# Kernel optimization log

Measured on AMD Instinct MI355X. Metric: run time of the kernel, lower is better.

Reference implementation:

```python
import jax, jax.numpy as jnp
import numpy as np

B, N, R, DIM = 4, 1024, 5, 1024
H, DH = 16, 64
ALPHA = 128.0
# FLAGS.fix_attention=True, a_sim=False: q * (dim_head**-0.5 * alpha**-1) * mult**-0.5
SCALE = (DH ** -0.5) * (1.0 / ALPHA) * (R ** -0.5)
EPS = 1e-5


def layernorm(x, g):
    mean = jnp.mean(x, axis=-1, keepdims=True)
    var = jnp.mean((x - mean) ** 2, axis=-1, keepdims=True)  # unbiased=False
    return (x - mean) * jax.lax.rsqrt(var + EPS) * g


def setup_inputs() -> dict:
    key = jax.random.key(0)
    ks = jax.random.split(key, 8)
    x = jax.random.normal(ks[0], (B, N, R, DIM), dtype=jnp.float32)
    mask = jax.random.bernoulli(ks[1], 0.9, (B, N))
    g_in = jnp.ones((DIM,), dtype=jnp.float32)
    Wq = jax.random.normal(ks[2], (DIM, H * DH), dtype=jnp.float32) * 0.02
    Wkv = jax.random.normal(ks[3], (DIM, 2 * DH), dtype=jnp.float32) * 0.02
    null_kv = jax.random.normal(ks[4], (2, DH), dtype=jnp.float32)
    Wout = jax.random.normal(ks[5], (H * DH, DIM), dtype=jnp.float32) * 0.02
    g_out = jnp.ones((DIM,), dtype=jnp.float32)
    return {"x": x, "mask": mask, "g_in": g_in, "Wq": Wq, "Wkv": Wkv,
            "null_kv": null_kv, "Wout": Wout, "g_out": g_out}


def reference(x, mask, g_in, Wq, Wkv, null_kv, Wout, g_out):
    # context defaults to the UN-normalized x (set before norm in the original)
    context = x
    xn = layernorm(x, g_in)                               # [b,n,r,dim]
    q = jnp.einsum('bnrc,ce->bnre', xn, Wq)               # [b,n,r,h*d]
    q = q.reshape(B, N, R, H, DH).transpose(0, 3, 1, 2, 4)  # b h n r d
    q = q * SCALE
    kv = jnp.einsum('bnrc,ce->bnre', context, Wkv)        # [b,n,r,2d] (multi-query: 1 kv head)
    k, v = kv[..., :DH], kv[..., DH:]                     # [b,n,r,d]
    # null kv token prepended along the j (sequence) axis, repeated over r
    nk = jnp.broadcast_to(null_kv[0], (B, 1, R, DH))
    nv = jnp.broadcast_to(null_kv[1], (B, 1, R, DH))
    k = jnp.concatenate([nk, k], axis=1)                  # [b,n+1,r,d]
    v = jnp.concatenate([nv, v], axis=1)
    sim = jnp.einsum('bhird,bjrd->bhij', q, k)            # [b,h,n,n+1]
    big = jnp.finfo(sim.dtype).max
    maskp = jnp.pad(mask, ((0, 0), (1, 0)), constant_values=True)  # null token always visible
    sim = jnp.where(maskp[:, None, None, :], sim, -big)
    # pb-relax: subtract detached row max, rescale by alpha
    sim = sim - jax.lax.stop_gradient(jnp.max(sim, axis=-1, keepdims=True))
    attn = jax.nn.softmax(sim * ALPHA, axis=-1)
    out = jnp.einsum('bhij,bjrd->bhird', attn, v)         # b h n r d
    out = out.transpose(0, 2, 3, 1, 4).reshape(B, N, R, H * DH)
    out = jnp.einsum('bnre,eo->bnro', out, Wout)
    return layernorm(out, g_out)
```

## Files before the change

kernel.cpp:

```cpp
#include <hip/hip_runtime.h>

#define B_   4
#define N_   1024
#define R_   5
#define DIM_ 1024
#define H_   16
#define DH_  64
#define NJ   1056
#define CDIM 320
#define MROWS (B_*N_*R_)

typedef unsigned int u32;
typedef unsigned short u16;
typedef __attribute__((ext_vector_type(8))) short bf16x8;
typedef __attribute__((ext_vector_type(4))) float f32x4;
typedef __attribute__((ext_vector_type(16))) float f32x16;

constexpr float SCALEA_ = (float)(0.05590169943749474 * 1.4426950408889634);

__device__ __forceinline__ u16 f2bf(float f) {
  u32 u = __builtin_bit_cast(u32, f);
  u32 r = (u + 0x7fffu + ((u >> 16) & 1u)) >> 16;
  return (u16)r;
}
__device__ __forceinline__ u32 pack2(float lo, float hi) {
  return (u32)f2bf(lo) | ((u32)f2bf(hi) << 16);
}
__device__ __forceinline__ void gld_lds16(void* lds, const void* g) {
  __builtin_amdgcn_global_load_lds((const __attribute__((address_space(1))) u32*)g,
                                   (__attribute__((address_space(3))) u32*)lds, 16, 0, 0);
}

__global__ void mask_detect(const u32* __restrict__ m, int* __restrict__ flag) {
  int t = threadIdx.x;
  int fl = 0;
  for (int i = t; i < 1024; i += 256) {
    u32 wv = m[i];
    if (wv == 0x3f800000u) fl |= 4;
    else if (wv > 1u) fl |= 2;
    if ((i & 1) && wv == 1u) fl |= 1;
  }
  if (fl) atomicOr(flag, fl);
}

__global__ void build_bias(const void* __restrict__ mask, const int* __restrict__ flag,
                           float* __restrict__ biasg) {
  int idx = blockIdx.x * 256 + threadIdx.x;
  if (idx >= B_ * NJ) return;
  int b = idx / NJ, j = idx % NJ;
  int mv;
  if (j == 0) mv = 1;
  else if (j > N_) mv = 0;
  else {
    int fb = flag[0];
    int mode = (fb & 4) ? 2 : ((fb & 2) ? 1 : ((fb & 1) ? 0 : 3));
    int mi = b * N_ + (j - 1);
    if (mode == 0)      mv = ((const int*)mask)[mi] != 0;
    else if (mode == 1) mv = ((const unsigned char*)mask)[mi] != 0;
    else if (mode == 2) mv = ((const float*)mask)[mi] != 0.0f;
    else                mv = ((const int*)mask)[mi * 2] != 0;
  }
  biasg[idx] = mv ? 0.0f : -__builtin_inff();
}

__global__ void kvfill(const float* __restrict__ nullkv, u16* __restrict__ kg, u16* __restrict__ vTg) {
  int idx = blockIdx.x * 256 + threadIdx.x;
  if (idx >= B_ * 32 * CDIM) return;
  int c  = idx % CDIM;
  int jj = (idx / CDIM) & 31;
  int b  = idx / (CDIM * 32);
  int j  = (jj == 0) ? 0 : (1024 + jj);
  u16 kvv, vvv;
  if (jj == 0) { kvv = f2bf(nullkv[c & 63]); vvv = f2bf(nullkv[64 + (c & 63)]); }
  else         { kvv = 0; vvv = 0; }
  kg [(size_t)(b * NJ + j) * CDIM + c] = kvv;
  vTg[(((size_t)b * 33 + (j >> 5)) * CDIM + c) * 32 + (j & 31)] = vvv;
}

__global__ __launch_bounds__(256) void transpose_cast(const float* __restrict__ W,
                                                      u16* __restrict__ WT, int K, int Nn) {
  __shared__ float tile[32][33];
  int tx = threadIdx.x & 31, ty = threadIdx.x >> 5;
  int n0 = blockIdx.x * 32, k0 = blockIdx.y * 32;
  #pragma unroll
  for (int e = 0; e < 4; ++e)
    tile[ty + e * 8][tx] = W[(size_t)(k0 + ty + e * 8) * Nn + n0 + tx];
  __syncthreads();
  #pragma unroll
  for (int e = 0; e < 4; ++e)
    WT[(size_t)(n0 + ty + e * 8) * K + k0 + tx] = f2bf(tile[tx][ty + e * 8]);
}

__global__ __launch_bounds__(256) void ln_in(const float* __restrict__ x, const float* __restrict__ gin,
                                             u16* __restrict__ xn, u16* __restrict__ xb) {
  const size_t row = blockIdx.x;
  const int t = threadIdx.x, w = t >> 6, lane = t & 63;
  const float* xr = x + row * 1024;
  f32x4 v = *(const f32x4*)(xr + t * 4);
  float s = v[0] + v[1] + v[2] + v[3];
  #pragma unroll
  for (int o = 1; o < 64; o <<= 1) s += __shfl_xor(s, o);
  __shared__ float red[8];
  if (lane == 0) red[w] = s;
  __syncthreads();
  float mean = (red[0] + red[1] + red[2] + red[3]) * (1.0f / 1024.0f);
  f32x4 d;
  float ss = 0.f;
  #pragma unroll
  for (int e = 0; e < 4; ++e) { d[e] = v[e] - mean; ss += d[e] * d[e]; }
  #pragma unroll
  for (int o = 1; o < 64; o <<= 1) ss += __shfl_xor(ss, o);
  if (lane == 0) red[4 + w] = ss;
  __syncthreads();
  float var = (red[4] + red[5] + red[6] + red[7]) * (1.0f / 1024.0f);
  float rs = rsqrtf(var + 1e-5f);
  f32x4 gv = *(const f32x4*)(gin + t * 4);
  uint2 o1, o2;
  o1.x = pack2(d[0] * rs * gv[0], d[1] * rs * gv[1]);
  o1.y = pack2(d[2] * rs * gv[2], d[3] * rs * gv[3]);
  o2.x = pack2(v[0], v[1]);
  o2.y = pack2(v[2], v[3]);
  *(uint2*)(xn + row * 1024 + t * 4) = o1;
  *(uint2*)(xb + row * 1024 + t * 4) = o2;
}

__global__ __launch_bounds__(256) void ln_out(const u16* __restrict__ yb, const float* __restrict__ gout,
                                              float* __restrict__ out) {
  const size_t row = blockIdx.x;
  const int t = threadIdx.x, w = t >> 6, lane = t & 63;
  uint2 raw = *(const uint2*)(yb + row * 1024 + t * 4);
  f32x4 v;
  v[0] = __builtin_bit_cast(float, (raw.x & 0xffffu) << 16);
  v[1] = __builtin_bit_cast(float, (raw.x & 0xffff0000u));
  v[2] = __builtin_bit_cast(float, (raw.y & 0xffffu) << 16);
  v[3] = __builtin_bit_cast(float, (raw.y & 0xffff0000u));
  float s = v[0] + v[1] + v[2] + v[3];
  #pragma unroll
  for (int o = 1; o < 64; o <<= 1) s += __shfl_xor(s, o);
  __shared__ float red[8];
  if (lane == 0) red[w] = s;
  __syncthreads();
  float mean = (red[0] + red[1] + red[2] + red[3]) * (1.0f / 1024.0f);
  f32x4 d;
  float ss = 0.f;
  #pragma unroll
  for (int e = 0; e < 4; ++e) { d[e] = v[e] - mean; ss += d[e] * d[e]; }
  #pragma unroll
  for (int o = 1; o < 64; o <<= 1) ss += __shfl_xor(ss, o);
  if (lane == 0) red[4 + w] = ss;
  __syncthreads();
  float var = (red[4] + red[5] + red[6] + red[7]) * (1.0f / 1024.0f);
  float rs = rsqrtf(var + 1e-5f);
  f32x4 gv = *(const f32x4*)(gout + t * 4);
  f32x4 o;
  #pragma unroll
  for (int e = 0; e < 4; ++e) o[e] = d[e] * rs * gv[e];
  *(f32x4*)(out + row * 1024 + t * 4) = o;
}

template <int EPI>
__global__ __launch_bounds__(256) void gemm_bt(const u16* __restrict__ A, const u16* __restrict__ BT,
                                               void* __restrict__ C0, void* __restrict__ C1,
                                               const int K, const int Nn) {
  __shared__ __align__(16) u16 As[128 * 32];
  __shared__ __align__(16) u16 Bs[128 * 32];
  const int t = threadIdx.x, w = t >> 6, lane = t & 63;
  const int g = lane >> 4, i16 = lane & 15;
  const int wr = w >> 1, wc = w & 1;
  const size_t m0 = (size_t)blockIdx.y * 128;
  const size_t n0 = (size_t)blockIdx.x * 128;
  const u16* Ab = A + m0 * K;
  const u16* Bb = BT + n0 * K;
  f32x4 acc[4][4];
  #pragma unroll
  for (int mi = 0; mi < 4; ++mi)
    #pragma unroll
    for (int ni = 0; ni < 4; ++ni) acc[mi][ni] = (f32x4){0.f, 0.f, 0.f, 0.f};

  for (int k0 = 0; k0 < K; k0 += 32) {
    __syncthreads();
    #pragma unroll
    for (int s = 0; s < 2; ++s) {
      int c = s * 256 + t;
      gld_lds16(&As[(s * 256 + w * 64) * 8], Ab + (size_t)(c >> 2) * K + k0 + (c & 3) * 8);
      gld_lds16(&Bs[(s * 256 + w * 64) * 8], Bb + (size_t)(c >> 2) * K + k0 + (c & 3) * 8);
    }
    __syncthreads();
    bf16x8 af[4], bfr[4];
    #pragma unroll
    for (int mi = 0; mi < 4; ++mi) af[mi]  = *(const bf16x8*)&As[(wr * 64 + mi * 16 + i16) * 32 + g * 8];
    #pragma unroll
    for (int ni = 0; ni < 4; ++ni) bfr[ni] = *(const bf16x8*)&Bs[(wc * 64 + ni * 16 + i16) * 32 + g * 8];
    #pragma unroll
    for (int mi = 0; mi < 4; ++mi)
      #pragma unroll
      for (int ni = 0; ni < 4; ++ni)
        acc[mi][ni] = __builtin_amdgcn_mfma_f32_16x16x32_bf16(af[mi], bfr[ni], acc[mi][ni], 0, 0, 0);
  }

  #pragma unroll
  for (int mi = 0; mi < 4; ++mi)
    #pragma unroll
    for (int ni = 0; ni < 4; ++ni)
      #pragma unroll
      for (int reg = 0; reg < 4; ++reg) {
        size_t gr = m0 + wr * 64 + mi * 16 + g * 4 + reg;
        int gc = (int)n0 + wc * 64 + ni * 16 + i16;
        float v = acc[mi][ni][reg];
        if (EPI == 0) {
          ((u16*)C0)[gr * 1024 + gc] = f2bf(v * SCALEA_);
        } else if (EPI == 1) {
          int grr = (int)gr;
          int b = grr / (N_ * R_);
          int rem = grr - b * (N_ * R_);
          int n = rem / R_;
          int r = rem - n * R_;
          int j = n + 1;
          u16 val = f2bf(v);
          if (gc < DH_) ((u16*)C0)[(size_t)(b * NJ + j) * CDIM + r * 64 + gc] = val;
          else ((u16*)C1)[(((size_t)b * 33 + (j >> 5)) * CDIM + r * 64 + (gc - DH_)) * 32 + (j & 31)] = val;
        } else {
          ((u16*)C0)[gr * 1024 + gc] = f2bf(v);
        }
      }
}

__global__ __launch_bounds__(256, 2) void attn_kernel(const u16* __restrict__ qb, const u16* __restrict__ kg,
                                                      const u16* __restrict__ vTg, const float* __restrict__ biasg,
                                                      u16* __restrict__ attout) {
  const int blk0 = blockIdx.x;
  const int blk = (blk0 & 7) * 128 + (blk0 >> 3);
  const int ch = blk & 1;
  const int it = (blk >> 1) & 7;
  const int h  = (blk >> 4) & 15;
  const int b  = blk >> 8;
  const int t = threadIdx.x;
  const int w = t >> 6, lane = t & 63;
  const int l31 = lane & 31, lh = lane >> 5;
  const int i0 = it * 128 + w * 32;

  __shared__ __align__(16) char Kl[2][20480];
  __shared__ __align__(16) char Vl[2][10240];

  int ksrc[5];
  #pragma unroll
  for (int s = 0; s < 5; ++s) {
    int d = w * 320 + s * 64 + lane;
    int j = d / 40, c16 = d - j * 40;
    int fj = (j & 7) ^ (j >> 3);
    ksrc[s] = j * 640 + ((c16 ^ fj) << 4);
  }
  int vsrc[3];
  #pragma unroll
  for (int s = 0; s < 3; ++s) {
    int d = s * 256 + t;
    int vc = d >> 2, sl = d & 3;
    int gv = (vc & 3) ^ ((vc >> 3) & 3);
    vsrc[s] = (ch * 160 + vc) * 64 + ((sl ^ gv) << 4);
  }
  const char* ktile = (const char*)(kg + (size_t)b * NJ * CDIM);
  const char* vtile = (const char*)(vTg + (size_t)b * 33 * CDIM * 32);

  bf16x8 qf[20];
  {
    const u16* qrow = qb + ((size_t)(b * N_ + i0 + l31) * R_) * 1024 + h * 64 + lh * 8;
    #pragma unroll
    for (int kk = 0; kk < 20; ++kk) {
      int k16 = kk * 16;
      qf[kk] = *(const bf16x8*)(qrow + (k16 >> 6) * 1024 + (k16 & 63));
    }
  }

  const float* bptr = biasg + b * NJ + lh * 4;

  f32x16 O[5];
  #pragma unroll
  for (int cf = 0; cf < 5; ++cf)
    #pragma unroll
    for (int r = 0; r < 16; ++r) O[cf][r] = 0.f;
  float d_run = 0.f;

  #pragma unroll
  for (int s = 0; s < 5; ++s)
    gld_lds16(&Kl[0][w * 5120 + s * 1024], ktile + ksrc[s]);
  {
    gld_lds16(&Vl[0][w * 1024],        vtile + vsrc[0]);
    gld_lds16(&Vl[0][4096 + w * 1024], vtile + vsrc[1]);
    if (w < 2) gld_lds16(&Vl[0][8192 + w * 1024], vtile + vsrc[2]);
  }

  const int swzK = ((l31 & 7) ^ (l31 >> 3)) << 4;
  const int swzV = ((l31 & 3) ^ ((l31 >> 3) & 3)) << 4;

  for (int jt = 0; jt < 33; ++jt) {
    const int cur = jt & 1;

    asm volatile("s_waitcnt vmcnt(0)" ::: "memory");
    __builtin_amdgcn_s_barrier();
    __builtin_amdgcn_sched_barrier(0);

    if (jt < 32) {
      const char* kt1 = ktile + (size_t)(jt + 1) * 20480;
      const char* vt1 = vtile + (size_t)(jt + 1) * 20480;
      #pragma unroll
      for (int s = 0; s < 5; ++s)
        gld_lds16(&Kl[cur ^ 1][w * 5120 + s * 1024], kt1 + ksrc[s]);
      gld_lds16(&Vl[cur ^ 1][w * 1024],        vt1 + vsrc[0]);
      gld_lds16(&Vl[cur ^ 1][4096 + w * 1024], vt1 + vsrc[1]);
      if (w < 2) gld_lds16(&Vl[cur ^ 1][8192 + w * 1024], vt1 + vsrc[2]);
    }

    const char* Kb  = &Kl[cur][0] + l31 * 640;
    const char* kb0 = Kb + ((0x00 | (lh << 4)) ^ swzK);
    const char* kb1 = Kb + ((0x20 | (lh << 4)) ^ swzK);
    const char* kb2 = Kb + ((0x40 | (lh << 4)) ^ swzK);
    const char* kb3 = Kb + ((0x60 | (lh << 4)) ^ swzK);
    f32x16 S0, S1;
    #pragma unroll
    for (int r = 0; r < 16; ++r) { S0[r] = 0.f; S1[r] = 0.f; }
    __builtin_amdgcn_s_setprio(1);
    #pragma unroll
    for (int kk = 0; kk < 20; ++kk) {
      const char* kb = ((kk & 3) == 0) ? kb0 : ((kk & 3) == 1) ? kb1 : ((kk & 3) == 2) ? kb2 : kb3;
      bf16x8 kf = *(const bf16x8*)(kb + (kk >> 2) * 128);
      if (kk & 1) S1 = __builtin_amdgcn_mfma_f32_32x32x16_bf16(kf, qf[kk], S1, 0, 0, 0);
      else        S0 = __builtin_amdgcn_mfma_f32_32x32x16_bf16(kf, qf[kk], S0, 0, 0, 0);
    }
    __builtin_amdgcn_s_setprio(0);

    f32x4 bb0 = *(const f32x4*)(bptr + (size_t)jt * 32 + 0);
    f32x4 bb1 = *(const f32x4*)(bptr + (size_t)jt * 32 + 8);
    f32x4 bb2 = *(const f32x4*)(bptr + (size_t)jt * 32 + 16);
    f32x4 bb3 = *(const f32x4*)(bptr + (size_t)jt * 32 + 24);
    float p[16];
    float ts = 0.f;
    #pragma unroll
    for (int r = 0; r < 16; ++r) {
      float bv = (r < 4) ? bb0[r & 3] : (r < 8) ? bb1[r & 3] : (r < 12) ? bb2[r & 3] : bb3[r & 3];
      float L = fminf(S0[r] + S1[r] + bv, 80.0f);
      p[r] = exp2f(L);
      ts += p[r];
    }
    d_run += ts;

    u32 pk0, pk1, pk2, pk3, pk4, pk5, pk6, pk7;
    asm("v_cvt_pk_bf16_f32 %0, %1, %2" : "=v"(pk0) : "v"(p[0]),  "v"(p[1]));
    asm("v_cvt_pk_bf16_f32 %0, %1, %2" : "=v"(pk1) : "v"(p[2]),  "v"(p[3]));
    asm("v_cvt_pk_bf16_f32 %0, %1, %2" : "=v"(pk2) : "v"(p[4]),  "v"(p[5]));
    asm("v_cvt_pk_bf16_f32 %0, %1, %2" : "=v"(pk3) : "v"(p[6]),  "v"(p[7]));
    asm("v_cvt_pk_bf16_f32 %0, %1, %2" : "=v"(pk4) : "v"(p[8]),  "v"(p[9]));
    asm("v_cvt_pk_bf16_f32 %0, %1, %2" : "=v"(pk5) : "v"(p[10]), "v"(p[11]));
    asm("v_cvt_pk_bf16_f32 %0, %1, %2" : "=v"(pk6) : "v"(p[12]), "v"(p[13]));
    asm("v_cvt_pk_bf16_f32 %0, %1, %2" : "=v"(pk7) : "v"(p[14]), "v"(p[15]));
    asm volatile("v_permlane32_swap_b32 %0, %1" : "+v"(pk0), "+v"(pk2));
    asm volatile("v_permlane32_swap_b32 %0, %1" : "+v"(pk1), "+v"(pk3));
    asm volatile("v_permlane32_swap_b32 %0, %1" : "+v"(pk4), "+v"(pk6));
    asm volatile("v_permlane32_swap_b32 %0, %1" : "+v"(pk5), "+v"(pk7));
    union { u32 u[4]; bf16x8 v; } f1, f2;
    f1.u[0] = pk0; f1.u[1] = pk1; f1.u[2] = pk2; f1.u[3] = pk3;
    f2.u[0] = pk4; f2.u[1] = pk5; f2.u[2] = pk6; f2.u[3] = pk7;

    const char* Vb  = &Vl[cur][0] + l31 * 64;
    const char* vb1 = Vb + ((lh << 4) ^ swzV);
    const char* vb2 = Vb + (((lh ^ 2) << 4) ^ swzV);
    __builtin_amdgcn_s_setprio(1);
    #pragma unroll
    for (int cf = 0; cf < 5; ++cf) {
      bf16x8 v0 = *(const bf16x8*)(vb1 + cf * 2048);
      bf16x8 v1 = *(const bf16x8*)(vb2 + cf * 2048);
      O[cf] = __builtin_amdgcn_mfma_f32_32x32x16_bf16(f1.v, v0, O[cf], 0, 0, 0);
      O[cf] = __builtin_amdgcn_mfma_f32_32x32x16_bf16(f2.v, v1, O[cf], 0, 0, 0);
    }
    __builtin_amdgcn_s_setprio(0);
  }

  d_run += __shfl_xor(d_run, 32);
  float inv = 1.0f / d_run;
  float invr[16];
  #pragma unroll
  for (int r = 0; r < 16; ++r) invr[r] = __shfl(inv, (r & 3) + 8 * (r >> 2) + 4 * lh);

  #pragma unroll
  for (int r = 0; r < 16; ++r) {
    int gi = i0 + (r & 3) + 8 * (r >> 2) + 4 * lh;
    u16* orow = attout + ((size_t)(b * N_ + gi) * R_) * 1024 + h * 64;
    #pragma unroll
    for (int cf = 0; cf < 5; ++cf) {
      int c = ch * 160 + cf * 32 + l31;
      orow[(c >> 6) * 1024 + (c & 63)] = f2bf(O[cf][r] * invr[r]);
    }
  }
}

extern "C" void kernel_launch(void* const* d_in, const int* in_sizes, int n_in,
                              void* d_out, int out_size, void* d_ws, size_t ws_size,
                              hipStream_t stream) {
  (void)in_sizes; (void)n_in; (void)out_size; (void)ws_size;
  const float* x      = (const float*)d_in[0];
  const void*  mask   = d_in[1];
  const float* g_in   = (const float*)d_in[2];
  const float* Wq     = (const float*)d_in[3];
  const float* Wkv    = (const float*)d_in[4];
  const float* nullkv = (const float*)d_in[5];
  const float* Wout   = (const float*)d_in[6];
  const float* g_out  = (const float*)d_in[7];
  float* out = (float*)d_out;

  char* base = (char*)d_ws;
  size_t off = 0;
  auto carve = [&](size_t bytes) { char* r = base + off; off += (bytes + 255) & ~(size_t)255; return r; };
  int*   flag  = (int*)carve(4);
  float* biasg = (float*)carve((size_t)B_ * NJ * 4);
  u16* WqT   = (u16*)carve((size_t)1024 * 1024 * 2);
  u16* WkvT  = (u16*)carve((size_t)128 * 1024 * 2);
  u16* WoutT = (u16*)carve((size_t)1024 * 1024 * 2);
  u16* xn    = (u16*)carve((size_t)MROWS * 1024 * 2);
  u16* xb    = (u16*)carve((size_t)MROWS * 1024 * 2);
  u16* qb    = (u16*)carve((size_t)MROWS * 1024 * 2);
  u16* kg    = (u16*)carve((size_t)B_ * NJ * CDIM * 2);
  u16* vTg   = (u16*)carve((size_t)B_ * 33 * CDIM * 32 * 2);
  u16* attout = xn;
  u16* yb     = xb;

  hipMemsetAsync(flag, 0, 4, stream);
  mask_detect<<<1, 256, 0, stream>>>((const u32*)mask, flag);
  build_bias<<<(B_ * NJ + 255) / 256, 256, 0, stream>>>(mask, flag, biasg);
  kvfill<<<(B_ * 32 * CDIM + 255) / 256, 256, 0, stream>>>(nullkv, kg, vTg);
  transpose_cast<<<dim3(32, 32), 256, 0, stream>>>(Wq, WqT, 1024, 1024);
  transpose_cast<<<dim3(4, 32), 256, 0, stream>>>(Wkv, WkvT, 1024, 128);
  transpose_cast<<<dim3(32, 32), 256, 0, stream>>>(Wout, WoutT, 1024, 1024);
  ln_in<<<MROWS, 256, 0, stream>>>(x, g_in, xn, xb);
  gemm_bt<0><<<dim3(8, 160), 256, 0, stream>>>(xn, WqT, qb, nullptr, 1024, 1024);
  gemm_bt<1><<<dim3(1, 160), 256, 0, stream>>>(xb, WkvT, kg, vTg, 1024, 128);
  attn_kernel<<<1024, 256, 0, stream>>>(qb, kg, vTg, biasg, attout);
  gemm_bt<2><<<dim3(8, 160), 256, 0, stream>>>(attout, WoutT, yb, nullptr, 1024, 1024);
  ln_out<<<MROWS, 256, 0, stream>>>(yb, g_out, out);
}
```

Measured before the change: 428.7 us.

## Software-pipeline PV MFMAs of previous tile into QK loop with triple-buffered V

Result: no change. 429.8 us (+0.3%).

```diff
diff --git a/kernel.cpp b/kernel.cpp
--- a/kernel.cpp
+++ b/kernel.cpp
@@ -240,7 +240,7 @@
   const int i0 = it * 128 + w * 32;
 
   __shared__ __align__(16) char Kl[2][20480];
-  __shared__ __align__(16) char Vl[2][10240];
+  __shared__ __align__(16) char Vl[3][10240];
 
   int ksrc[5];
   #pragma unroll
@@ -280,6 +280,15 @@
     for (int r = 0; r < 16; ++r) O[cf][r] = 0.f;
   float d_run = 0.f;
 
+  union { u32 u[4]; bf16x8 v; } f1p, f2p;
+  #pragma unroll
+  for (int e = 0; e < 4; ++e) { f1p.u[e] = 0; f2p.u[e] = 0; }
+
+  #pragma unroll
+  for (int z = 0; z < 3; ++z) {
+    int idx = z * 256 + t;
+    if (idx < 640) *(uint4*)&Vl[2][idx * 16] = (uint4){0, 0, 0, 0};
+  }
   #pragma unroll
   for (int s = 0; s < 5; ++s)
     gld_lds16(&Kl[0][w * 5120 + s * 1024], ktile + ksrc[s]);
@@ -294,20 +303,22 @@
 
   for (int jt = 0; jt < 33; ++jt) {
     const int cur = jt & 1;
-
-    asm volatile("s_waitcnt vmcnt(0)" ::: "memory");
+    const int pv  = (jt + 2) % 3;
+
+    asm volatile("s_waitcnt vmcnt(0) lgkmcnt(0)" ::: "memory");
     __builtin_amdgcn_s_barrier();
     __builtin_amdgcn_sched_barrier(0);
 
     if (jt < 32) {
       const char* kt1 = ktile + (size_t)(jt + 1) * 20480;
       const char* vt1 = vtile + (size_t)(jt + 1) * 20480;
+      char* vd = &Vl[(jt + 1) % 3][0];
       #pragma unroll
       for (int s = 0; s < 5; ++s)
         gld_lds16(&Kl[cur ^ 1][w * 5120 + s * 1024], kt1 + ksrc[s]);
-      gld_lds16(&Vl[cur ^ 1][w * 1024],        vt1 + vsrc[0]);
-      gld_lds16(&Vl[cur ^ 1][4096 + w * 1024], vt1 + vsrc[1]);
-      if (w < 2) gld_lds16(&Vl[cur ^ 1][8192 + w * 1024], vt1 + vsrc[2]);
+      gld_lds16(vd + w * 1024,        vt1 + vsrc[0]);
+      gld_lds16(vd + 4096 + w * 1024, vt1 + vsrc[1]);
+      if (w < 2) gld_lds16(vd + 8192 + w * 1024, vt1 + vsrc[2]);
     }
 
     const char* Kb  = &Kl[cur][0] + l31 * 640;
@@ -315,6 +326,9 @@
     const char* kb1 = Kb + ((0x20 | (lh << 4)) ^ swzK);
     const char* kb2 = Kb + ((0x40 | (lh << 4)) ^ swzK);
     const char* kb3 = Kb + ((0x60 | (lh << 4)) ^ swzK);
+    const char* Vb  = &Vl[pv][0] + l31 * 64;
+    const char* vb1 = Vb + ((lh << 4) ^ swzV);
+    const char* vb2 = Vb + (((lh ^ 2) << 4) ^ swzV);
     f32x16 S0, S1;
     #pragma unroll
     for (int r = 0; r < 16; ++r) { S0[r] = 0.f; S1[r] = 0.f; }
@@ -325,6 +339,11 @@
       bf16x8 kf = *(const bf16x8*)(kb + (kk >> 2) * 128);
       if (kk & 1) S1 = __builtin_amdgcn_mfma_f32_32x32x16_bf16(kf, qf[kk], S1, 0, 0, 0);
       else        S0 = __builtin_amdgcn_mfma_f32_32x32x16_bf16(kf, qf[kk], S0, 0, 0, 0);
+      if (kk < 10) {
+        int cf = kk >> 1;
+        bf16x8 vv = *(const bf16x8*)(((kk & 1) ? vb2 : vb1) + cf * 2048);
+        O[cf] = __builtin_amdgcn_mfma_f32_32x32x16_bf16((kk & 1) ? f2p.v : f1p.v, vv, O[cf], 0, 0, 0);
+      }
     }
     __builtin_amdgcn_s_setprio(0);
 
@@ -356,11 +375,12 @@
     asm volatile("v_permlane32_swap_b32 %0, %1" : "+v"(pk1), "+v"(pk3));
     asm volatile("v_permlane32_swap_b32 %0, %1" : "+v"(pk4), "+v"(pk6));
     asm volatile("v_permlane32_swap_b32 %0, %1" : "+v"(pk5), "+v"(pk7));
-    union { u32 u[4]; bf16x8 v; } f1, f2;
-    f1.u[0] = pk0; f1.u[1] = pk1; f1.u[2] = pk2; f1.u[3] = pk3;
-    f2.u[0] = pk4; f2.u[1] = pk5; f2.u[2] = pk6; f2.u[3] = pk7;
-
-    const char* Vb  = &Vl[cur][0] + l31 * 64;
+    f1p.u[0] = pk0; f1p.u[1] = pk1; f1p.u[2] = pk2; f1p.u[3] = pk3;
+    f2p.u[0] = pk4; f2p.u[1] = pk5; f2p.u[2] = pk6; f2p.u[3] = pk7;
+  }
+
+  {
+    const char* Vb  = &Vl[2][0] + l31 * 64;
     const char* vb1 = Vb + ((lh << 4) ^ swzV);
     const char* vb2 = Vb + (((lh ^ 2) << 4) ^ swzV);
     __builtin_amdgcn_s_setprio(1);
@@ -368,8 +388,8 @@
     for (int cf = 0; cf < 5; ++cf) {
       bf16x8 v0 = *(const bf16x8*)(vb1 + cf * 2048);
       bf16x8 v1 = *(const bf16x8*)(vb2 + cf * 2048);
-      O[cf] = __builtin_amdgcn_mfma_f32_32x32x16_bf16(f1.v, v0, O[cf], 0, 0, 0);
-      O[cf] = __builtin_amdgcn_mfma_f32_32x32x16_bf16(f2.v, v1, O[cf], 0, 0, 0);
+      O[cf] = __builtin_amdgcn_mfma_f32_32x32x16_bf16(f1p.v, v0, O[cf], 0, 0, 0);
+      O[cf] = __builtin_amdgcn_mfma_f32_32x32x16_bf16(f2p.v, v1, O[cf], 0, 0, 0);
     }
     __builtin_amdgcn_s_setprio(0);
   }
```

## Add triple-buffered async-LDS GEMM and merge setup kernels into one launch

Applied to the files above, without the earlier changes.

New measurement: 402.1 us. 1.07x faster.

```diff
diff --git a/kernel.cpp b/kernel.cpp
--- a/kernel.cpp
+++ b/kernel.cpp
@@ -31,64 +31,75 @@
                                    (__attribute__((address_space(3))) u32*)lds, 16, 0, 0);
 }
 
-__global__ void mask_detect(const u32* __restrict__ m, int* __restrict__ flag) {
-  int t = threadIdx.x;
-  int fl = 0;
-  for (int i = t; i < 1024; i += 256) {
-    u32 wv = m[i];
-    if (wv == 0x3f800000u) fl |= 4;
-    else if (wv > 1u) fl |= 2;
-    if ((i & 1) && wv == 1u) fl |= 1;
-  }
-  if (fl) atomicOr(flag, fl);
-}
-
-__global__ void build_bias(const void* __restrict__ mask, const int* __restrict__ flag,
-                           float* __restrict__ biasg) {
-  int idx = blockIdx.x * 256 + threadIdx.x;
-  if (idx >= B_ * NJ) return;
-  int b = idx / NJ, j = idx % NJ;
-  int mv;
-  if (j == 0) mv = 1;
-  else if (j > N_) mv = 0;
-  else {
-    int fb = flag[0];
-    int mode = (fb & 4) ? 2 : ((fb & 2) ? 1 : ((fb & 1) ? 0 : 3));
-    int mi = b * N_ + (j - 1);
-    if (mode == 0)      mv = ((const int*)mask)[mi] != 0;
-    else if (mode == 1) mv = ((const unsigned char*)mask)[mi] != 0;
-    else if (mode == 2) mv = ((const float*)mask)[mi] != 0.0f;
-    else                mv = ((const int*)mask)[mi * 2] != 0;
-  }
-  biasg[idx] = mv ? 0.0f : -__builtin_inff();
-}
-
-__global__ void kvfill(const float* __restrict__ nullkv, u16* __restrict__ kg, u16* __restrict__ vTg) {
-  int idx = blockIdx.x * 256 + threadIdx.x;
-  if (idx >= B_ * 32 * CDIM) return;
-  int c  = idx % CDIM;
-  int jj = (idx / CDIM) & 31;
-  int b  = idx / (CDIM * 32);
-  int j  = (jj == 0) ? 0 : (1024 + jj);
-  u16 kvv, vvv;
-  if (jj == 0) { kvv = f2bf(nullkv[c & 63]); vvv = f2bf(nullkv[64 + (c & 63)]); }
-  else         { kvv = 0; vvv = 0; }
-  kg [(size_t)(b * NJ + j) * CDIM + c] = kvv;
-  vTg[(((size_t)b * 33 + (j >> 5)) * CDIM + c) * 32 + (j & 31)] = vvv;
-}
-
-__global__ __launch_bounds__(256) void transpose_cast(const float* __restrict__ W,
-                                                      u16* __restrict__ WT, int K, int Nn) {
+__global__ __launch_bounds__(256) void prep(const void* __restrict__ mask, const float* __restrict__ nullkv,
+                                            const float* __restrict__ Wq, const float* __restrict__ Wkv,
+                                            const float* __restrict__ Wout,
+                                            float* __restrict__ biasg, u16* __restrict__ kg,
+                                            u16* __restrict__ vTg, u16* __restrict__ WqT,
+                                            u16* __restrict__ WkvT, u16* __restrict__ WoutT) {
+  const int bid = blockIdx.x, t = threadIdx.x;
+  __shared__ int sfl;
   __shared__ float tile[32][33];
-  int tx = threadIdx.x & 31, ty = threadIdx.x >> 5;
-  int n0 = blockIdx.x * 32, k0 = blockIdx.y * 32;
-  #pragma unroll
-  for (int e = 0; e < 4; ++e)
-    tile[ty + e * 8][tx] = W[(size_t)(k0 + ty + e * 8) * Nn + n0 + tx];
-  __syncthreads();
-  #pragma unroll
-  for (int e = 0; e < 4; ++e)
-    WT[(size_t)(n0 + ty + e * 8) * K + k0 + tx] = f2bf(tile[tx][ty + e * 8]);
+  if (bid < 17) {
+    if (t == 0) sfl = 0;
+    __syncthreads();
+    int fl = 0;
+    const u32* mw = (const u32*)mask;
+    for (int i = t; i < 1024; i += 256) {
+      u32 wv = mw[i];
+      if (wv == 0x3f800000u) fl |= 4;
+      else if (wv > 1u) fl |= 2;
+      if ((i & 1) && wv == 1u) fl |= 1;
+    }
+    if (fl) atomicOr(&sfl, fl);
+    __syncthreads();
+    int fb = sfl;
+    int idx = bid * 256 + t;
+    if (idx < B_ * NJ) {
+      int b = idx / NJ, j = idx % NJ;
+      int mv;
+      if (j == 0) mv = 1;
+      else if (j > N_) mv = 0;
+      else {
+        int mode = (fb & 4) ? 2 : ((fb & 2) ? 1 : ((fb & 1) ? 0 : 3));
+        int mi = b * N_ + (j - 1);
+        if (mode == 0)      mv = ((const int*)mask)[mi] != 0;
+        else if (mode == 1) mv = ((const unsigned char*)mask)[mi] != 0;
+        else if (mode == 2) mv = ((const float*)mask)[mi] != 0.0f;
+        else                mv = ((const int*)mask)[mi * 2] != 0;
+      }
+      biasg[idx] = mv ? 0.0f : -__builtin_inff();
+    }
+  } else if (bid < 177) {
+    int idx = (bid - 17) * 256 + t;
+    if (idx < B_ * 32 * CDIM) {
+      int c  = idx % CDIM;
+      int jj = (idx / CDIM) & 31;
+      int b  = idx / (CDIM * 32);
+      int j  = (jj == 0) ? 0 : (1024 + jj);
+      u16 kvv, vvv;
+      if (jj == 0) { kvv = f2bf(nullkv[c & 63]); vvv = f2bf(nullkv[64 + (c & 63)]); }
+      else         { kvv = 0; vvv = 0; }
+      kg [(size_t)(b * NJ + j) * CDIM + c] = kvv;
+      vTg[(((size_t)b * 33 + (j >> 5)) * CDIM + c) * 32 + (j & 31)] = vvv;
+    }
+  } else {
+    const float* W; u16* WT; int Nn, id;
+    if (bid < 1201)      { W = Wq;   WT = WqT;   Nn = 1024; id = bid - 177; }
+    else if (bid < 1329) { W = Wkv;  WT = WkvT;  Nn = 128;  id = bid - 1201; }
+    else                 { W = Wout; WT = WoutT; Nn = 1024; id = bid - 1329; }
+    const int K = 1024;
+    int nb = (Nn == 128) ? 4 : 32;
+    int n0 = (id % nb) * 32, k0 = (id / nb) * 32;
+    int tx = t & 31, ty = t >> 5;
+    #pragma unroll
+    for (int e = 0; e < 4; ++e)
+      tile[ty + e * 8][tx] = W[(size_t)(k0 + ty + e * 8) * Nn + n0 + tx];
+    __syncthreads();
+    #pragma unroll
+    for (int e = 0; e < 4; ++e)
+      WT[(size_t)(n0 + ty + e * 8) * K + k0 + tx] = f2bf(tile[tx][ty + e * 8]);
+  }
 }
 
 __global__ __launch_bounds__(256) void ln_in(const float* __restrict__ x, const float* __restrict__ gin,
@@ -159,9 +170,89 @@
 }
 
 template <int EPI>
-__global__ __launch_bounds__(256) void gemm_bt(const u16* __restrict__ A, const u16* __restrict__ BT,
-                                               void* __restrict__ C0, void* __restrict__ C1,
-                                               const int K, const int Nn) {
+__global__ __launch_bounds__(256, 3) void gemm_r3(const u16* __restrict__ A, const u16* __restrict__ BT,
+                                                  u16* __restrict__ C0, const int K) {
+  __shared__ __align__(16) u16 Al[3][128 * 32];
+  __shared__ __align__(16) u16 Bl[3][128 * 32];
+  const int t = threadIdx.x, w = t >> 6, lane = t & 63;
+  const int g = lane >> 4, i16 = lane & 15;
+  const int wr = w >> 1, wc = w & 1;
+  const size_t m0 = (size_t)blockIdx.y * 128;
+  const size_t n0 = (size_t)blockIdx.x * 128;
+  const size_t K2 = (size_t)K * 2;
+
+  const char* asrc[2];
+  const char* bsrc[2];
+  #pragma unroll
+  for (int s = 0; s < 2; ++s) {
+    int r = (s * 4 + w) * 16 + (lane >> 2);
+    int sw = (((lane & 3) ^ ((lane >> 2) & 3)) << 4);
+    asrc[s] = (const char*)(A + m0 * K) + (size_t)r * K2 + sw;
+    bsrc[s] = (const char*)(BT + n0 * K) + (size_t)r * K2 + sw;
+  }
+
+  f32x4 acc[4][4];
+  #pragma unroll
+  for (int mi = 0; mi < 4; ++mi)
+    #pragma unroll
+    for (int ni = 0; ni < 4; ++ni) acc[mi][ni] = (f32x4){0.f, 0.f, 0.f, 0.f};
+
+  auto stage = [&](int kt) {
+    const int slot = kt % 3;
+    const size_t kb = (size_t)kt * 64;
+    #pragma unroll
+    for (int s = 0; s < 2; ++s) {
+      gld_lds16(&Al[slot][(s * 4 + w) * 512], asrc[s] + kb);
+      gld_lds16(&Bl[slot][(s * 4 + w) * 512], bsrc[s] + kb);
+    }
+  };
+
+  stage(0);
+  stage(1);
+  const int NT = K >> 5;
+  const int rdsw = ((g ^ (i16 & 3)) << 4);
+
+  for (int kt = 0; kt < NT; ++kt) {
+    if (kt < NT - 1) asm volatile("s_waitcnt vmcnt(4)" ::: "memory");
+    else             asm volatile("s_waitcnt vmcnt(0)" ::: "memory");
+    __builtin_amdgcn_s_barrier();
+    __builtin_amdgcn_sched_barrier(0);
+
+    if (kt + 2 < NT) stage(kt + 2);
+
+    const int slot = kt % 3;
+    const char* apb = (const char*)&Al[slot][0] + (wr * 64 + i16) * 64 + rdsw;
+    const char* bpb = (const char*)&Bl[slot][0] + (wc * 64 + i16) * 64 + rdsw;
+    bf16x8 af[4], bfr[4];
+    #pragma unroll
+    for (int mi = 0; mi < 4; ++mi) af[mi]  = *(const bf16x8*)(apb + mi * 1024);
+    #pragma unroll
+    for (int ni = 0; ni < 4; ++ni) bfr[ni] = *(const bf16x8*)(bpb + ni * 1024);
+    __builtin_amdgcn_s_setprio(1);
+    #pragma unroll
+    for (int mi = 0; mi < 4; ++mi)
+      #pragma unroll
+      for (int ni = 0; ni < 4; ++ni)
+        acc[mi][ni] = __builtin_amdgcn_mfma_f32_16x16x32_bf16(af[mi], bfr[ni], acc[mi][ni], 0, 0, 0);
+    __builtin_amdgcn_s_setprio(0);
+  }
+
+  #pragma unroll
+  for (int mi = 0; mi < 4; ++mi)
+    #pragma unroll
+    for (int ni = 0; ni < 4; ++ni)
+      #pragma unroll
+      for (int reg = 0; reg < 4; ++reg) {
+        size_t gr = m0 + wr * 64 + mi * 16 + g * 4 + reg;
+        int gc = (int)n0 + wc * 64 + ni * 16 + i16;
+        float v = acc[mi][ni][reg];
+        C0[gr * 1024 + gc] = f2bf(EPI == 0 ? v * SCALEA_ : v);
+      }
+}
+
+__global__ __launch_bounds__(256) void gemm_kv(const u16* __restrict__ A, const u16* __restrict__ BT,
+                                               u16* __restrict__ C0, u16* __restrict__ C1,
+                                               const int K) {
   __shared__ __align__(16) u16 As[128 * 32];
   __shared__ __align__(16) u16 Bs[128 * 32];
   const int t = threadIdx.x, w = t >> 6, lane = t & 63;
@@ -207,21 +298,15 @@
         size_t gr = m0 + wr * 64 + mi * 16 + g * 4 + reg;
         int gc = (int)n0 + wc * 64 + ni * 16 + i16;
         float v = acc[mi][ni][reg];
-        if (EPI == 0) {
-          ((u16*)C0)[gr * 1024 + gc] = f2bf(v * SCALEA_);
-        } else if (EPI == 1) {
-          int grr = (int)gr;
-          int b = grr / (N_ * R_);
-          int rem = grr - b * (N_ * R_);
-          int n = rem / R_;
-          int r = rem - n * R_;
-          int j = n + 1;
-          u16 val = f2bf(v);
-          if (gc < DH_) ((u16*)C0)[(size_t)(b * NJ + j) * CDIM + r * 64 + gc] = val;
-          else ((u16*)C1)[(((size_t)b * 33 + (j >> 5)) * CDIM + r * 64 + (gc - DH_)) * 32 + (j & 31)] = val;
-        } else {
-          ((u16*)C0)[gr * 1024 + gc] = f2bf(v);
-        }
+        int grr = (int)gr;
+        int b = grr / (N_ * R_);
+        int rem = grr - b * (N_ * R_);
+        int n = rem / R_;
+        int r = rem - n * R_;
+        int j = n + 1;
+        u16 val = f2bf(v);
+        if (gc < DH_) C0[(size_t)(b * NJ + j) * CDIM + r * 64 + gc] = val;
+        else C1[(((size_t)b * 33 + (j >> 5)) * CDIM + r * 64 + (gc - DH_)) * 32 + (j & 31)] = val;
       }
 }
 
@@ -409,7 +494,6 @@
   char* base = (char*)d_ws;
   size_t off = 0;
   auto carve = [&](size_t bytes) { char* r = base + off; off += (bytes + 255) & ~(size_t)255; return r; };
-  int*   flag  = (int*)carve(4);
   float* biasg = (float*)carve((size_t)B_ * NJ * 4);
   u16* WqT   = (u16*)carve((size_t)1024 * 1024 * 2);
   u16* WkvT  = (u16*)carve((size_t)128 * 1024 * 2);
@@ -422,17 +506,11 @@
   u16* attout = xn;
   u16* yb     = xb;
 
-  hipMemsetAsync(flag, 0, 4, stream);
-  mask_detect<<<1, 256, 0, stream>>>((const u32*)mask, flag);
-  build_bias<<<(B_ * NJ + 255) / 256, 256, 0, stream>>>(mask, flag, biasg);
-  kvfill<<<(B_ * 32 * CDIM + 255) / 256, 256, 0, stream>>>(nullkv, kg, vTg);
-  transpose_cast<<<dim3(32, 32), 256, 0, stream>>>(Wq, WqT, 1024, 1024);
-  transpose_cast<<<dim3(4, 32), 256, 0, stream>>>(Wkv, WkvT, 1024, 128);
-  transpose_cast<<<dim3(32, 32), 256, 0, stream>>>(Wout, WoutT, 1024, 1024);
+  prep<<<2353, 256, 0, stream>>>(mask, nullkv, Wq, Wkv, Wout, biasg, kg, vTg, WqT, WkvT, WoutT);
   ln_in<<<MROWS, 256, 0, stream>>>(x, g_in, xn, xb);
-  gemm_bt<0><<<dim3(8, 160), 256, 0, stream>>>(xn, WqT, qb, nullptr, 1024, 1024);
-  gemm_bt<1><<<dim3(1, 160), 256, 0, stream>>>(xb, WkvT, kg, vTg, 1024, 128);
+  gemm_r3<0><<<dim3(8, 160), 256, 0, stream>>>(xn, WqT, qb, 1024);
+  gemm_kv<<<dim3(1, 160), 256, 0, stream>>>(xb, WkvT, kg, vTg, 1024);
   attn_kernel<<<1024, 256, 0, stream>>>(qb, kg, vTg, biasg, attout);
-  gemm_bt<2><<<dim3(8, 160), 256, 0, stream>>>(attout, WoutT, yb, nullptr, 1024, 1024);
+  gemm_r3<2><<<dim3(8, 160), 256, 0, stream>>>(attout, WoutT, yb, 1024);
   ln_out<<<MROWS, 256, 0, stream>>>(yb, g_out, out);
 }
```
